# Optimization experiments

Hardware: AMD Instinct MI355X
Metric: run time of the kernel (lower is better)

Reference implementation:

```python
import jax, jax.numpy as jnp
import numpy as np

B, T, C = 8, 2048, 1024
NEG = -1e30  # stand-in for -inf in the stable-softmax running max


def setup_inputs() -> dict:
    key = jax.random.key(0)
    ks = jax.random.split(key, 5)
    x = jax.random.normal(ks[0], (B, T, C), dtype=jnp.float32)
    scales = jnp.arange(C, dtype=jnp.float32) / C  # matches init_weight()
    Wk = jax.random.normal(ks[1], (C, C), dtype=jnp.float32) * 0.02
    Wv = jax.random.normal(ks[2], (C, C), dtype=jnp.float32) * 0.02
    Wr = jax.random.normal(ks[3], (C, C), dtype=jnp.float32) * 0.02
    Wo = jax.random.normal(ks[4], (C, C), dtype=jnp.float32) * 0.02
    return {
        'x': x,
        'w': scales, 'u': scales,
        'mix_k': scales, 'mix_v': scales, 'mix_r': scales,
        'Wk': Wk, 'Wv': Wv, 'Wr': Wr, 'Wo': Wo,
    }


def wkv(w, u, k, v):
    # Numerically-stable RWKV WKV recurrence. k, v: [B, T, C]; w, u: [C]
    w_exp = -jnp.exp(w)  # per-channel log-decay (negative)
    p0 = jnp.zeros(k.shape[::2], k.dtype)      # [B, C] numerator state
    q0 = jnp.zeros(k.shape[::2], k.dtype)      # [B, C] denominator state
    o0 = jnp.full(k.shape[::2], NEG, k.dtype)  # [B, C] running max (log-space)

    def step(carry, kv_t):
        p, q, o = carry
        k_t, v_t = kv_t  # each [B, C]
        uk = u + k_t
        no = jnp.maximum(o, uk)
        A = jnp.exp(o - no)
        Bc = jnp.exp(uk - no)
        out = (A * p + Bc * v_t) / (A * q + Bc)
        wo = w_exp + o
        no2 = jnp.maximum(wo, k_t)
        A2 = jnp.exp(wo - no2)
        B2 = jnp.exp(k_t - no2)
        return (A2 * p + B2 * v_t, A2 * q + B2, no2), out

    kT = jnp.swapaxes(k, 0, 1)  # [T, B, C]
    vT = jnp.swapaxes(v, 0, 1)
    _, outs = jax.lax.scan(step, (p0, q0, o0), (kT, vT))
    return jnp.swapaxes(outs, 0, 1)  # [B, T, C]


def reference(x, w, u, mix_k, mix_v, mix_r, Wk, Wv, Wr, Wo):
    # time_shift: ZeroPad2d((0,0,1,-1)) => shift sequence right by one, zero-pad front
    x_prev = jnp.pad(x, ((0, 0), (1, 0), (0, 0)))[:, :-1]
    # torch.lerp(start=x_prev, end=x, weight=mix)
    xk = x_prev + mix_k * (x - x_prev)
    xv = x_prev + mix_v * (x - x_prev)
    xr = x_prev + mix_r * (x - x_prev)
    k = jnp.einsum('btc,dc->btd', xk, Wk)
    v = jnp.einsum('btc,dc->btd', xv, Wv)
    sr = jax.nn.sigmoid(jnp.einsum('btc,dc->btd', xr, Wr))
    rwkv = sr * wkv(w, u, k, v)
    return jnp.einsum('btc,dc->btd', rwkv, Wo)
```

## Files before the change

### kernel.cpp

```cpp
#include <hip/hip_runtime.h>
#include <hip/hip_bf16.h>
#include <stdint.h>

#define Bb   8
#define Tt   2048
#define Cdim 1024
#define BT   16384
#define SLAB ((size_t)BT * Cdim)

#define NC   32
#define LCH  64
#define CSUB 32

typedef __attribute__((ext_vector_type(4))) float f32x4;
typedef __attribute__((ext_vector_type(8))) short bf16x8;

__device__ inline short f2bs(float f) {
    union { __hip_bfloat16 h; short s; } u;
    u.h = __float2bfloat16(f);
    return u.s;
}
__device__ inline float bs2f(short s) {
    union { short s; __hip_bfloat16 h; } u;
    u.s = s;
    return __bfloat162float(u.h);
}

#define GLOAD_LDS16(g, l) __builtin_amdgcn_global_load_lds( \
    (const __attribute__((address_space(1))) void*)(g),     \
    (__attribute__((address_space(3))) void*)(l), 16, 0, 0)

#define SBAR()      __builtin_amdgcn_s_barrier()

__global__ __launch_bounds__(256) void prep_all(
    const float* __restrict__ x,
    const float* __restrict__ mk,
    const float* __restrict__ mv,
    const float* __restrict__ mr,
    const float* __restrict__ Wk, const float* __restrict__ Wv,
    const float* __restrict__ Wr, const float* __restrict__ Wo,
    short* __restrict__ xmix,
    short* __restrict__ wbf)
{
    int bid = blockIdx.x;
    if (bid < 8192) {
        int idx = bid * 256 + threadIdx.x;
        int c8  = idx & (Cdim / 8 - 1);
        int m   = idx >> 7;
        int c0  = c8 << 3;
        int t   = m & (Tt - 1);

        float xs[8], ps[8];
        const float4* xp = (const float4*)(x + (size_t)m * Cdim + c0);
        float4 xa = xp[0], xb = xp[1];
        xs[0]=xa.x; xs[1]=xa.y; xs[2]=xa.z; xs[3]=xa.w;
        xs[4]=xb.x; xs[5]=xb.y; xs[6]=xb.z; xs[7]=xb.w;
        if (t != 0) {
            const float4* pp = (const float4*)(x + (size_t)(m - 1) * Cdim + c0);
            float4 pa = pp[0], pb = pp[1];
            ps[0]=pa.x; ps[1]=pa.y; ps[2]=pa.z; ps[3]=pa.w;
            ps[4]=pb.x; ps[5]=pb.y; ps[6]=pb.z; ps[7]=pb.w;
        } else {
            #pragma unroll
            for (int j = 0; j < 8; ++j) ps[j] = 0.f;
        }

        const float* mixes[3] = {mk, mv, mr};
        #pragma unroll
        for (int z = 0; z < 3; ++z) {
            const float4* mp = (const float4*)(mixes[z] + c0);
            float4 ma = mp[0], mb = mp[1];
            float mm[8];
            mm[0]=ma.x; mm[1]=ma.y; mm[2]=ma.z; mm[3]=ma.w;
            mm[4]=mb.x; mm[5]=mb.y; mm[6]=mb.z; mm[7]=mb.w;
            bf16x8 o;
            #pragma unroll
            for (int j = 0; j < 8; ++j)
                o[j] = f2bs(ps[j] + mm[j] * (xs[j] - ps[j]));
            *(bf16x8*)(xmix + (size_t)z * SLAB + (size_t)m * Cdim + c0) = o;
        }
    } else {
        int idx = (bid - 8192) * 256 + threadIdx.x;
        int z   = idx >> 17;
        int r   = idx & (Cdim * Cdim / 8 - 1);
        const float* src = (z == 0) ? Wk : (z == 1) ? Wv : (z == 2) ? Wr : Wo;
        const float4* sp = (const float4*)(src + (size_t)r * 8);
        float4 a = sp[0], b = sp[1];
        float v[8] = {a.x, a.y, a.z, a.w, b.x, b.y, b.z, b.w};
        bf16x8 o;
        #pragma unroll
        for (int j = 0; j < 8; ++j) o[j] = f2bs(v[j]);
        *(bf16x8*)(wbf + (size_t)z * Cdim * Cdim + (size_t)r * 8) = o;
    }
}

template<int FUSED>
__global__ __launch_bounds__(512, 2) void gemm256(
    const short* __restrict__ Abase,
    const short* __restrict__ Wbase,
    void* __restrict__ o0, void* __restrict__ o1)
{
    __shared__ __align__(16) char lds[131072];

    const int tid  = threadIdx.x;
    const int lane = tid & 63;
    const int wv   = tid >> 6;
    const int wm   = wv >> 2, wn = wv & 3;
    const int NT   = Cdim / 64;

    int orig = blockIdx.y * (FUSED ? 12 : 4) + blockIdx.x;
    int xcd  = orig & 7;
    int s    = orig >> 3;
    int z, nt, yt;
    if (FUSED) {
        z  = s >> 5;
        int rem = s & 31;
        nt = rem & 3;
        yt = xcd * 8 + (rem >> 2);
    } else {
        z  = 0;
        nt = s & 3;
        yt = xcd * 8 + (s >> 2);
    }

    const short* A  = Abase + (size_t)z * SLAB;
    const short* Bm = Wbase + (size_t)z * Cdim * Cdim;
    const int m0 = yt * 256;
    const int n0 = nt * 256;

    f32x4 acc[8][4] = {};

    const int lm = lane & 15, lq = lane >> 4, lb7 = lane & 7;
    int ck[2];
    #pragma unroll
    for (int ks = 0; ks < 2; ++ks) ck[ks] = (((ks * 4 + lq) ^ lb7) << 4);
    int aoff[8];
    #pragma unroll
    for (int i = 0; i < 8; ++i) aoff[i] = (i * 16 + lm) * 128;
    int boff[4];
    #pragma unroll
    for (int j = 0; j < 4; ++j) boff[j] = ((wn & 1) * 64 + j * 16 + lm) * 128;
    const int aReg = wm << 14;
    const int bReg = 32768 + ((wn >> 1) << 14);

    const int rlo  = tid >> 3;
    const int clog = (tid & 7) ^ (rlo & 7);
    auto STAGE = [&](int tt, int part) {
        const short* mat = (part < 2) ? A : Bm;
        int rb = ((part < 2) ? m0 : n0) + ((part & 1) << 7);
        const short* g0 = mat + (size_t)(rb + rlo)      * Cdim + (tt << 6) + (clog << 3);
        const short* g1 = mat + (size_t)(rb + 64 + rlo) * Cdim + (tt << 6) + (clog << 3);
        char* l = lds + ((tt & 1) << 16) + (part << 14) + tid * 16;
        GLOAD_LDS16(g0, l);
        GLOAD_LDS16(g1, l + 8192);
    };

    STAGE(0, 0); STAGE(0, 1); STAGE(0, 2); STAGE(0, 3);
    STAGE(1, 0); STAGE(1, 1);
    asm volatile("s_waitcnt vmcnt(4)" ::: "memory");
    SBAR();

    bf16x8 a0[4][2], a4[4][2], b01[2][2], b23[2][2];

    #pragma unroll 1
    for (int kt = 0; kt < NT; ++kt) {
        const char* base = lds + ((kt & 1) << 16);

        #pragma unroll
        for (int i = 0; i < 4; ++i)
            #pragma unroll
            for (int ks = 0; ks < 2; ++ks)
                a0[i][ks] = *(const bf16x8*)(base + aReg + aoff[i] + ck[ks]);
        #pragma unroll
        for (int j = 0; j < 2; ++j)
            #pragma unroll
            for (int ks = 0; ks < 2; ++ks)
                b01[j][ks] = *(const bf16x8*)(base + bReg + boff[j] + ck[ks]);
        #pragma unroll
        for (int i = 0; i < 4; ++i)
            #pragma unroll
            for (int ks = 0; ks < 2; ++ks)
                a4[i][ks] = *(const bf16x8*)(base + aReg + aoff[i + 4] + ck[ks]);
        #pragma unroll
        for (int j = 0; j < 2; ++j)
            #pragma unroll
            for (int ks = 0; ks < 2; ++ks)
                b23[j][ks] = *(const bf16x8*)(base + bReg + boff[j + 2] + ck[ks]);
        if (kt + 1 < NT) { STAGE(kt + 1, 2); STAGE(kt + 1, 3); }
        __builtin_amdgcn_s_setprio(1);
        #pragma unroll
        for (int ks = 0; ks < 2; ++ks)
            #pragma unroll
            for (int i = 0; i < 4; ++i)
                #pragma unroll
                for (int j = 0; j < 2; ++j)
                    acc[i][j] = __builtin_amdgcn_mfma_f32_16x16x32_bf16(
                        a0[i][ks], b01[j][ks], acc[i][j], 0, 0, 0);
        #pragma unroll
        for (int ks = 0; ks < 2; ++ks)
            #pragma unroll
            for (int i = 0; i < 4; ++i)
                #pragma unroll
                for (int j = 0; j < 2; ++j)
                    acc[i + 4][j] = __builtin_amdgcn_mfma_f32_16x16x32_bf16(
                        a4[i][ks], b01[j][ks], acc[i + 4][j], 0, 0, 0);
        __builtin_amdgcn_s_setprio(0);
        SBAR();

        if (kt + 2 < NT) { STAGE(kt + 2, 0); STAGE(kt + 2, 1); }
        __builtin_amdgcn_s_setprio(1);
        #pragma unroll
        for (int ks = 0; ks < 2; ++ks)
            #pragma unroll
            for (int i = 0; i < 4; ++i)
                #pragma unroll
                for (int j = 0; j < 2; ++j)
                    acc[i + 4][j + 2] = __builtin_amdgcn_mfma_f32_16x16x32_bf16(
                        a4[i][ks], b23[j][ks], acc[i + 4][j + 2], 0, 0, 0);
        #pragma unroll
        for (int ks = 0; ks < 2; ++ks)
            #pragma unroll
            for (int i = 0; i < 4; ++i)
                #pragma unroll
                for (int j = 0; j < 2; ++j)
                    acc[i][j + 2] = __builtin_amdgcn_mfma_f32_16x16x32_bf16(
                        a0[i][ks], b23[j][ks], acc[i][j + 2], 0, 0, 0);
        __builtin_amdgcn_s_setprio(0);
        if      (kt + 2 < NT) { asm volatile("s_waitcnt vmcnt(4)" ::: "memory"); }
        else if (kt + 1 < NT) { asm volatile("s_waitcnt vmcnt(0)" ::: "memory"); }
        SBAR();
    }

    int col0 = n0 + wn * 64 + lm;
    int row0 = m0 + wm * 128 + (lq << 2);
    #pragma unroll
    for (int i = 0; i < 8; ++i) {
        #pragma unroll
        for (int j = 0; j < 4; ++j) {
            #pragma unroll
            for (int r = 0; r < 4; ++r) {
                int row = row0 + i * 16 + r;
                int cc  = col0 + j * 16;
                float vvv = acc[i][j][r];
                if (FUSED) {
                    if (z == 2) {
                        ((short*)o1)[(size_t)row * Cdim + cc] =
                            f2bs(1.f / (1.f + __expf(-vvv)));
                    } else {
                        ((short*)o0)[((size_t)row * Cdim + cc) * 2 + z] = f2bs(vvv);
                    }
                } else {
                    ((float*)o0)[(size_t)row * Cdim + cc] = vvv;
                }
            }
        }
    }
}

__global__ __launch_bounds__(1024) void wkv_chunked(
    const int* __restrict__ kv, const short* __restrict__ srb,
    const float* __restrict__ w, const float* __restrict__ u,
    short* __restrict__ rwkv)
{
    __shared__ float sp[NC][CSUB];
    __shared__ float sq[NC][CSUB];
    __shared__ float so[NC][CSUB];

    int tid = threadIdx.x;
    int cl  = tid & (CSUB - 1);
    int ch  = tid >> 5;
    int b   = blockIdx.x >> 5;
    int cg  = blockIdx.x & 31;
    int c   = cg * CSUB + cl;

    float wexp = -__expf(w[c]);
    float uu   = u[c];
    size_t coff = (size_t)b * Tt * Cdim + (size_t)(ch * LCH) * Cdim + c;

    float p = 0.f, q = 0.f, o = -1e30f;
    #pragma unroll 8
    for (int t = 0; t < LCH; ++t) {
        size_t off = coff + (size_t)t * Cdim;
        int pk = kv[off];
        float kt = bs2f((short)(pk & 0xffff));
        float vt = bs2f((short)((unsigned)pk >> 16));
        float wo  = wexp + o;
        float no  = fmaxf(wo, kt);
        float A   = __expf(wo - no);
        float B2  = __expf(kt - no);
        p = A * p + B2 * vt;
        q = A * q + B2;
        o = no;
    }
    sp[ch][cl] = p; sq[ch][cl] = q; so[ch][cl] = o;
    __syncthreads();

    if (tid < CSUB) {
        float Ld = wexp * (float)LCH;
        float cp = 0.f, cq = 0.f, co = -1e30f;
        for (int j = 0; j < NC; ++j) {
            float lp = sp[j][tid], lq = sq[j][tid], lo = so[j][tid];
            sp[j][tid] = cp; sq[j][tid] = cq; so[j][tid] = co;
            float od = co + Ld;
            float no = fmaxf(od, lo);
            float A  = __expf(od - no);
            float B2 = __expf(lo - no);
            cp = A * cp + B2 * lp;
            cq = A * cq + B2 * lq;
            co = no;
        }
    }
    __syncthreads();

    p = sp[ch][cl]; q = sq[ch][cl]; o = so[ch][cl];
    #pragma unroll 8
    for (int t = 0; t < LCH; ++t) {
        size_t off = coff + (size_t)t * Cdim;
        int pk = kv[off];
        float kt = bs2f((short)(pk & 0xffff));
        float vt = bs2f((short)((unsigned)pk >> 16));
        float sr = bs2f(srb[off]);

        float uk  = uu + kt;
        float no  = fmaxf(o, uk);
        float Aa  = __expf(o - no);
        float Bc  = __expf(uk - no);
        float out = (Aa * p + Bc * vt) / (Aa * q + Bc);

        float wo  = wexp + o;
        float no2 = fmaxf(wo, kt);
        float A2  = __expf(wo - no2);
        float B2  = __expf(kt - no2);
        p = A2 * p + B2 * vt;
        q = A2 * q + B2;
        o = no2;

        rwkv[off] = f2bs(sr * out);
    }
}

extern "C" void kernel_launch(void* const* d_in, const int* in_sizes, int n_in,
                              void* d_out, int out_size, void* d_ws, size_t ws_size,
                              hipStream_t stream)
{
    const float* x    = (const float*)d_in[0];
    const float* w    = (const float*)d_in[1];
    const float* u    = (const float*)d_in[2];
    const float* mixk = (const float*)d_in[3];
    const float* mixv = (const float*)d_in[4];
    const float* mixr = (const float*)d_in[5];
    const float* Wk   = (const float*)d_in[6];
    const float* Wv   = (const float*)d_in[7];
    const float* Wr   = (const float*)d_in[8];
    const float* Wo   = (const float*)d_in[9];

    char* ws = (char*)d_ws;
    short* xmix = (short*)ws;
    short* wbf  = (short*)(ws + 3 * SLAB * 2);
    short* rbuf = (short*)(ws + 3 * SLAB * 2 + (size_t)4 * Cdim * Cdim * 2);
    short* rwkv = (short*)ws;
    int*   kvbf = (int*)d_out;

    prep_all<<<8192 + 2048, 256, 0, stream>>>(x, mixk, mixv, mixr,
                                              Wk, Wv, Wr, Wo, xmix, wbf);

    dim3 gf(12, BT / 256);
    gemm256<1><<<gf, 512, 0, stream>>>(xmix, wbf, kvbf, rbuf);

    wkv_chunked<<<Bb * (Cdim / CSUB), 1024, 0, stream>>>(kvbf, rbuf, w, u, rwkv);

    dim3 go(Cdim / 256, BT / 256);
    gemm256<0><<<go, 512, 0, stream>>>(rwkv, wbf + 3 * (size_t)Cdim * Cdim,
                                       (float*)d_out, nullptr);
}
```

Before: 235.5 us.

## Split k/v into separate bf16 planes and process two channels per WKV thread

The fused GEMM now writes k and v into separate bf16 arrays instead of an interleaved k/v int array. The WKV kernel has each thread handle two adjacent channels with 32-bit loads and stores, over 64 chunks of 32 timesteps instead of 32 chunks of 64. This widens memory accesses, doubles independent work per thread for ILP, and halves the serial chunk length. The cost is a longer serial cross-chunk scan (64 steps) run by only 16 threads, and the GEMM epilogue stores stay scalar 16-bit writes to the separate planes.

Measured after the change: 246.9 us. +4.9%, slower.

```diff
diff --git a/kernel.cpp b/kernel.cpp
--- a/kernel.cpp
+++ b/kernel.cpp
@@ -8,9 +8,8 @@
 #define BT   16384
 #define SLAB ((size_t)BT * Cdim)
 
-#define NC   32
-#define LCH  64
-#define CSUB 32
+#define NCb   64
+#define LCHb  32
 
 typedef __attribute__((ext_vector_type(4))) float f32x4;
 typedef __attribute__((ext_vector_type(8))) short bf16x8;
@@ -98,7 +97,7 @@
 __global__ __launch_bounds__(512, 2) void gemm256(
     const short* __restrict__ Abase,
     const short* __restrict__ Wbase,
-    void* __restrict__ o0, void* __restrict__ o1)
+    void* __restrict__ o0, void* __restrict__ o1, void* __restrict__ o2)
 {
     __shared__ __align__(16) char lds[131072];
 
@@ -243,12 +242,9 @@
                 int cc  = col0 + j * 16;
                 float vvv = acc[i][j][r];
                 if (FUSED) {
-                    if (z == 2) {
-                        ((short*)o1)[(size_t)row * Cdim + cc] =
-                            f2bs(1.f / (1.f + __expf(-vvv)));
-                    } else {
-                        ((short*)o0)[((size_t)row * Cdim + cc) * 2 + z] = f2bs(vvv);
-                    }
+                    short* outb = (short*)((z == 0) ? o0 : (z == 1) ? o1 : o2);
+                    if (z == 2) vvv = 1.f / (1.f + __expf(-vvv));
+                    outb[(size_t)row * Cdim + cc] = f2bs(vvv);
                 } else {
                     ((float*)o0)[(size_t)row * Cdim + cc] = vvv;
                 }
@@ -258,84 +254,97 @@
 }
 
 __global__ __launch_bounds__(1024) void wkv_chunked(
-    const int* __restrict__ kv, const short* __restrict__ srb,
+    const short* __restrict__ kb, const short* __restrict__ vb,
+    const short* __restrict__ srb,
     const float* __restrict__ w, const float* __restrict__ u,
     short* __restrict__ rwkv)
 {
-    __shared__ float sp[NC][CSUB];
-    __shared__ float sq[NC][CSUB];
-    __shared__ float so[NC][CSUB];
+    __shared__ float sp[NCb][32], sq[NCb][32], so[NCb][32];
 
     int tid = threadIdx.x;
-    int cl  = tid & (CSUB - 1);
-    int ch  = tid >> 5;
+    int pl  = tid & 15;
+    int ch  = tid >> 4;
     int b   = blockIdx.x >> 5;
     int cg  = blockIdx.x & 31;
-    int c   = cg * CSUB + cl;
-
-    float wexp = -__expf(w[c]);
-    float uu   = u[c];
-    size_t coff = (size_t)b * Tt * Cdim + (size_t)(ch * LCH) * Cdim + c;
-
-    float p = 0.f, q = 0.f, o = -1e30f;
+    int c0  = cg * 32 + pl * 2;
+
+    float w0 = -__expf(w[c0]),     w1 = -__expf(w[c0 + 1]);
+    float u0 = u[c0],              u1 = u[c0 + 1];
+    size_t coff = (size_t)b * Tt * Cdim + (size_t)(ch * LCHb) * Cdim + c0;
+
+    float p0 = 0.f, q0 = 0.f, o0 = -1e30f;
+    float p1 = 0.f, q1 = 0.f, o1 = -1e30f;
     #pragma unroll 8
-    for (int t = 0; t < LCH; ++t) {
+    for (int t = 0; t < LCHb; ++t) {
         size_t off = coff + (size_t)t * Cdim;
-        int pk = kv[off];
-        float kt = bs2f((short)(pk & 0xffff));
-        float vt = bs2f((short)((unsigned)pk >> 16));
-        float wo  = wexp + o;
-        float no  = fmaxf(wo, kt);
-        float A   = __expf(wo - no);
-        float B2  = __expf(kt - no);
-        p = A * p + B2 * vt;
-        q = A * q + B2;
-        o = no;
-    }
-    sp[ch][cl] = p; sq[ch][cl] = q; so[ch][cl] = o;
+        int kk = *(const int*)(kb + off);
+        int vv = *(const int*)(vb + off);
+        float k0 = bs2f((short)kk), k1 = bs2f((short)((unsigned)kk >> 16));
+        float v0 = bs2f((short)vv), v1 = bs2f((short)((unsigned)vv >> 16));
+        float wo0 = w0 + o0,            wo1 = w1 + o1;
+        float no0 = fmaxf(wo0, k0),     no1 = fmaxf(wo1, k1);
+        float A0  = __expf(wo0 - no0),  A1  = __expf(wo1 - no1);
+        float B0  = __expf(k0 - no0),   B1  = __expf(k1 - no1);
+        p0 = A0 * p0 + B0 * v0;         p1 = A1 * p1 + B1 * v1;
+        q0 = A0 * q0 + B0;              q1 = A1 * q1 + B1;
+        o0 = no0;                       o1 = no1;
+    }
+    sp[ch][pl * 2] = p0; sq[ch][pl * 2] = q0; so[ch][pl * 2] = o0;
+    sp[ch][pl * 2 + 1] = p1; sq[ch][pl * 2 + 1] = q1; so[ch][pl * 2 + 1] = o1;
     __syncthreads();
 
-    if (tid < CSUB) {
-        float Ld = wexp * (float)LCH;
-        float cp = 0.f, cq = 0.f, co = -1e30f;
-        for (int j = 0; j < NC; ++j) {
-            float lp = sp[j][tid], lq = sq[j][tid], lo = so[j][tid];
-            sp[j][tid] = cp; sq[j][tid] = cq; so[j][tid] = co;
-            float od = co + Ld;
-            float no = fmaxf(od, lo);
-            float A  = __expf(od - no);
-            float B2 = __expf(lo - no);
-            cp = A * cp + B2 * lp;
-            cq = A * cq + B2 * lq;
-            co = no;
+    if (tid < 16) {
+        int lcA = tid * 2, lcB = tid * 2 + 1;
+        float LdA = -__expf(w[cg * 32 + lcA]) * (float)LCHb;
+        float LdB = -__expf(w[cg * 32 + lcB]) * (float)LCHb;
+        float cpA = 0.f, cqA = 0.f, coA = -1e30f;
+        float cpB = 0.f, cqB = 0.f, coB = -1e30f;
+        for (int j = 0; j < NCb; ++j) {
+            float lpA = sp[j][lcA], lqA = sq[j][lcA], loA = so[j][lcA];
+            float lpB = sp[j][lcB], lqB = sq[j][lcB], loB = so[j][lcB];
+            sp[j][lcA] = cpA; sq[j][lcA] = cqA; so[j][lcA] = coA;
+            sp[j][lcB] = cpB; sq[j][lcB] = cqB; so[j][lcB] = coB;
+            float odA = coA + LdA,          odB = coB + LdB;
+            float noA = fmaxf(odA, loA),    noB = fmaxf(odB, loB);
+            float AA  = __expf(odA - noA),  AB  = __expf(odB - noB);
+            float BA  = __expf(loA - noA),  BB  = __expf(loB - noB);
+            cpA = AA * cpA + BA * lpA;      cpB = AB * cpB + BB * lpB;
+            cqA = AA * cqA + BA * lqA;      cqB = AB * cqB + BB * lqB;
+            coA = noA;                      coB = noB;
         }
     }
     __syncthreads();
 
-    p = sp[ch][cl]; q = sq[ch][cl]; o = so[ch][cl];
+    p0 = sp[ch][pl * 2]; q0 = sq[ch][pl * 2]; o0 = so[ch][pl * 2];
+    p1 = sp[ch][pl * 2 + 1]; q1 = sq[ch][pl * 2 + 1]; o1 = so[ch][pl * 2 + 1];
     #pragma unroll 8
-    for (int t = 0; t < LCH; ++t) {
+    for (int t = 0; t < LCHb; ++t) {
         size_t off = coff + (size_t)t * Cdim;
-        int pk = kv[off];
-        float kt = bs2f((short)(pk & 0xffff));
-        float vt = bs2f((short)((unsigned)pk >> 16));
-        float sr = bs2f(srb[off]);
-
-        float uk  = uu + kt;
-        float no  = fmaxf(o, uk);
-        float Aa  = __expf(o - no);
-        float Bc  = __expf(uk - no);
-        float out = (Aa * p + Bc * vt) / (Aa * q + Bc);
-
-        float wo  = wexp + o;
-        float no2 = fmaxf(wo, kt);
-        float A2  = __expf(wo - no2);
-        float B2  = __expf(kt - no2);
-        p = A2 * p + B2 * vt;
-        q = A2 * q + B2;
-        o = no2;
-
-        rwkv[off] = f2bs(sr * out);
+        int kk = *(const int*)(kb + off);
+        int vv = *(const int*)(vb + off);
+        int rr = *(const int*)(srb + off);
+        float k0 = bs2f((short)kk), k1 = bs2f((short)((unsigned)kk >> 16));
+        float v0 = bs2f((short)vv), v1 = bs2f((short)((unsigned)vv >> 16));
+        float s0 = bs2f((short)rr), s1 = bs2f((short)((unsigned)rr >> 16));
+
+        float uk0 = u0 + k0,            uk1 = u1 + k1;
+        float no0 = fmaxf(o0, uk0),     no1 = fmaxf(o1, uk1);
+        float Aa0 = __expf(o0 - no0),   Aa1 = __expf(o1 - no1);
+        float Bc0 = __expf(uk0 - no0),  Bc1 = __expf(uk1 - no1);
+        float out0 = (Aa0 * p0 + Bc0 * v0) / (Aa0 * q0 + Bc0);
+        float out1 = (Aa1 * p1 + Bc1 * v1) / (Aa1 * q1 + Bc1);
+
+        float wo0 = w0 + o0,            wo1 = w1 + o1;
+        float n20 = fmaxf(wo0, k0),     n21 = fmaxf(wo1, k1);
+        float A20 = __expf(wo0 - n20),  A21 = __expf(wo1 - n21);
+        float B20 = __expf(k0 - n20),   B21 = __expf(k1 - n21);
+        p0 = A20 * p0 + B20 * v0;       p1 = A21 * p1 + B21 * v1;
+        q0 = A20 * q0 + B20;            q1 = A21 * q1 + B21;
+        o0 = n20;                       o1 = n21;
+
+        unsigned lo = (unsigned short)f2bs(s0 * out0);
+        unsigned hi = (unsigned short)f2bs(s1 * out1);
+        *(unsigned*)(rwkv + off) = lo | (hi << 16);
     }
 }
 
@@ -359,17 +368,18 @@
     short* wbf  = (short*)(ws + 3 * SLAB * 2);
     short* rbuf = (short*)(ws + 3 * SLAB * 2 + (size_t)4 * Cdim * Cdim * 2);
     short* rwkv = (short*)ws;
-    int*   kvbf = (int*)d_out;
+    short* kbuf = (short*)d_out;
+    short* vbuf = kbuf + SLAB;
 
     prep_all<<<8192 + 2048, 256, 0, stream>>>(x, mixk, mixv, mixr,
                                               Wk, Wv, Wr, Wo, xmix, wbf);
 
     dim3 gf(12, BT / 256);
-    gemm256<1><<<gf, 512, 0, stream>>>(xmix, wbf, kvbf, rbuf);
-
-    wkv_chunked<<<Bb * (Cdim / CSUB), 1024, 0, stream>>>(kvbf, rbuf, w, u, rwkv);
+    gemm256<1><<<gf, 512, 0, stream>>>(xmix, wbf, kbuf, vbuf, rbuf);
+
+    wkv_chunked<<<Bb * (Cdim / 32), 1024, 0, stream>>>(kbuf, vbuf, rbuf, w, u, rwkv);
 
     dim3 go(Cdim / 256, BT / 256);
     gemm256<0><<<go, 512, 0, stream>>>(rwkv, wbf + 3 * (size_t)Cdim * Cdim,
-                                       (float*)d_out, nullptr);
-}
+                                       (float*)d_out, nullptr, nullptr);
+}
```
